# Kernel tuning notes

Measured on AMD Instinct MI355X. Metric: run time of the kernel, lower is better.

Reference implementation:

```python
import jax, jax.numpy as jnp
import numpy as np

B, S, D = 1, 2048, 4096
NH, NKV, HD = 32, 8, 128
ROPE_BASE = 500000.0
NEG = -1e30


def apply_rope(x):
    # x: [B, S, H, HD]; interleaved-pair rotary (Llama/torchtune style)
    pos = jnp.arange(x.shape[1], dtype=jnp.float32)
    inv_freq = ROPE_BASE ** (-jnp.arange(0, HD, 2, dtype=jnp.float32) / HD)  # [HD/2]
    ang = pos[:, None] * inv_freq[None, :]            # [S, HD/2]
    cos = jnp.cos(ang)[None, :, None, :]              # [1, S, 1, HD/2]
    sin = jnp.sin(ang)[None, :, None, :]
    xr = x.reshape(x.shape[0], x.shape[1], x.shape[2], HD // 2, 2)
    x0, x1 = xr[..., 0], xr[..., 1]
    out = jnp.stack([x0 * cos - x1 * sin, x0 * sin + x1 * cos], axis=-1)
    return out.reshape(x.shape).astype(x.dtype)


def setup_inputs() -> dict:
    key = jax.random.key(0)
    ks = jax.random.split(key, 5)
    sc = 1.0 / np.sqrt(D).astype(np.float32)
    return {
        "x": jax.random.normal(ks[0], (B, S, D), jnp.float32),
        "Wq": jax.random.normal(ks[1], (D, NH * HD), jnp.float32) * sc,
        "Wk": jax.random.normal(ks[2], (D, NKV * HD), jnp.float32) * sc,
        "Wv": jax.random.normal(ks[3], (D, NKV * HD), jnp.float32) * sc,
        "Wo": jax.random.normal(ks[4], (D, D), jnp.float32) * sc,
    }


def reference(x, Wq, Wk, Wv, Wo):
    # QKV projections (no bias; attention_bias=False)
    q = (x @ Wq).reshape(B, S, NH, HD)      # [B,S,NH,HD]
    k = (x @ Wk).reshape(B, S, NKV, HD)     # [B,S,NKV,HD]
    v = (x @ Wv).reshape(B, S, NKV, HD)
    # RoPE on q and k
    q = apply_rope(q)
    k = apply_rope(k)
    # GQA: group q heads over kv heads instead of materializing expanded k/v
    g = NH // NKV
    qg = q.reshape(B, S, NKV, g, HD)
    scale = 1.0 / np.sqrt(HD).astype(np.float32)
    scores = jnp.einsum('bsngh,btnh->bngst', qg, k) * scale  # [B,NKV,g,S,S]
    causal = jnp.tril(jnp.ones((S, S), dtype=bool))
    scores = jnp.where(causal, scores, NEG)
    p = jax.nn.softmax(scores, axis=-1)
    o = jnp.einsum('bngst,btnh->bsngh', p, v).reshape(B, S, NH * HD)
    return o @ Wo
```

## Files before the change

### kernel.cpp

```cpp
#include <hip/hip_runtime.h>
#include <cstdint>

#define S_LEN 2048
#define D_DIM 4096
#define NHEAD 32
#define NKVH  8
#define HDIM  128
#define NQKV  6144

typedef __bf16 bf16x8 __attribute__((ext_vector_type(8)));
typedef __bf16 bf16x2 __attribute__((ext_vector_type(2)));
typedef float floatx4 __attribute__((ext_vector_type(4)));
typedef unsigned short u16;
typedef unsigned int u32;

__device__ __forceinline__ u16 f2bf(float f) {
  u32 u = __builtin_bit_cast(u32, f);
  u += 0x7fffu + ((u >> 16) & 1u);
  return (u16)(u >> 16);
}
__device__ __forceinline__ float bf2f(u16 h) {
  u32 u = ((u32)h) << 16;
  return __builtin_bit_cast(float, u);
}
__device__ __forceinline__ u32 pack2(float a, float b) {
  bf16x2 t;
  t[0] = (__bf16)a;
  t[1] = (__bf16)b;
  return __builtin_bit_cast(u32, t);
}

__device__ __forceinline__ void gll16(const void* g, const void* l) {
  __builtin_amdgcn_global_load_lds(
      (const __attribute__((address_space(1))) u32*)(unsigned long long)(uintptr_t)g,
      (__attribute__((address_space(3))) u32*)(u32)(uintptr_t)l, 16, 0, 0);
}


__global__ __launch_bounds__(256) void prep_kernel(const float* __restrict__ x,
                                                   const float* __restrict__ Wq,
                                                   const float* __restrict__ Wk,
                                                   const float* __restrict__ Wv,
                                                   const float* __restrict__ Wo,
                                                   u16* __restrict__ x_bf,
                                                   u16* __restrict__ wqkvT,
                                                   u16* __restrict__ woT) {
  int id = blockIdx.x;
  if (id < 8192) {
    int i = (id * 256 + (int)threadIdx.x) * 4;
    float4 v = *(const float4*)(x + i);
    u32 lo = (u32)f2bf(v.x) | ((u32)f2bf(v.y) << 16);
    u32 hi = (u32)f2bf(v.z) | ((u32)f2bf(v.w) << 16);
    *(uint2*)(x_bf + i) = make_uint2(lo, hi);
    return;
  }
  id -= 8192;
  __shared__ float tile[64][65];
  const float* src;
  u16* dst;
  int N;
  if (id < 4096) {
    src = Wq; dst = wqkvT; N = 4096;
  } else if (id < 5120) {
    src = Wk; dst = wqkvT + (size_t)4096 * 4096; N = 1024; id -= 4096;
  } else if (id < 6144) {
    src = Wv; dst = wqkvT + (size_t)5120 * 4096; N = 1024; id -= 5120;
  } else {
    src = Wo; dst = woT; N = 4096; id -= 6144;
  }
  const int nb = id / 64, kb = id % 64;
  const int k0 = kb * 64, n0 = nb * 64;
  const int t = threadIdx.x;
  const int c4 = (t & 15) * 4, r0 = t >> 4;
#pragma unroll
  for (int p = 0; p < 4; ++p) {
    int r = r0 + p * 16;
    float4 v = *(const float4*)(src + (size_t)(k0 + r) * N + n0 + c4);
    tile[r][c4 + 0] = v.x;
    tile[r][c4 + 1] = v.y;
    tile[r][c4 + 2] = v.z;
    tile[r][c4 + 3] = v.w;
  }
  __syncthreads();
#pragma unroll
  for (int p = 0; p < 4; ++p) {
    int rr = r0 + p * 16;
    u32 a = (u32)f2bf(tile[c4 + 0][rr]) | ((u32)f2bf(tile[c4 + 1][rr]) << 16);
    u32 b = (u32)f2bf(tile[c4 + 2][rr]) | ((u32)f2bf(tile[c4 + 3][rr]) << 16);
    *(uint2*)(dst + (size_t)(n0 + rr) * 4096 + k0 + c4) = make_uint2(a, b);
  }
}


__global__ __launch_bounds__(256) void rope_vt_kernel(u16* __restrict__ qkv,
                                                      u16* __restrict__ vt) {
  int id = blockIdx.x;
  __shared__ u16 tile[64][65];
  if (id < 20480) {
    const int y = id >> 11, s = id & 2047;
    const int sub = threadIdx.x >> 6;
    const int i = threadIdx.x & 63;
    const int hh = y * 4 + sub;
    const int colbase = (hh < NHEAD) ? hh * HDIM : D_DIM + (hh - NHEAD) * HDIM;
    u32* p = (u32*)(qkv + (size_t)s * NQKV + colbase) + i;
    u32 pr = *p;
    float x0 = bf2f((u16)(pr & 0xffffu));
    float x1 = bf2f((u16)(pr >> 16));
    float invf = expf(-(float)(2 * i) * (13.122363377404328f / 128.0f));
    float ang = (float)s * invf;
    float cs = cosf(ang), sn = sinf(ang);
    float o0 = x0 * cs - x1 * sn;
    float o1 = x0 * sn + x1 * cs;
    *p = (u32)f2bf(o0) | ((u32)f2bf(o1) << 16);
    return;
  }
  const int vb = id - 20480;
  const int hk = vb >> 6;
  const int d0 = ((vb >> 5) & 1) * 64;
  const int s0 = (vb & 31) * 64;
  const int t = threadIdx.x, c = t & 63, r0 = t >> 6;
#pragma unroll
  for (int p = 0; p < 16; ++p) {
    int r = r0 + p * 4;
    tile[r][c] = qkv[(size_t)(s0 + r) * NQKV + 5120 + hk * HDIM + d0 + c];
  }
  __syncthreads();
#pragma unroll
  for (int p = 0; p < 16; ++p) {
    int rr = r0 + p * 4;
    vt[((size_t)hk * HDIM + d0 + rr) * S_LEN + s0 + c] = tile[c][rr];
  }
}


template <bool BF16_OUT>
__global__ __launch_bounds__(256) void gemm_bt(const u16* __restrict__ A,
                                               const u16* __restrict__ Bt,
                                               void* __restrict__ Cout,
                                               int M, int N, int K, int lda, int ldb) {
  __shared__ u16 As[2][128 * 32];
  __shared__ u16 Bs[2][128 * 32];
  const int tid = threadIdx.x;
  const int w = tid >> 6, lane = tid & 63;
  const int quad = lane >> 4, l15 = lane & 15;
  const int m0 = blockIdx.y * 128, n0 = blockIdx.x * 128;
  const int wm = (w & 1) * 64, wn = (w >> 1) * 64;
  floatx4 acc[4][4];
#pragma unroll
  for (int mi = 0; mi < 4; ++mi)
#pragma unroll
    for (int ni = 0; ni < 4; ++ni)
#pragma unroll
      for (int j = 0; j < 4; ++j) acc[mi][ni][j] = 0.0f;

  const int srow = w * 32 + (lane >> 2);
  const int kcol = (lane & 3) * 8;
  const u16* pA0 = A + (size_t)(m0 + srow) * lda + kcol;
  const u16* pA1 = pA0 + (size_t)16 * lda;
  const u16* pB0 = Bt + (size_t)(n0 + srow) * ldb + kcol;
  const u16* pB1 = pB0 + (size_t)16 * ldb;

  for (int k0 = 0; k0 < K; k0 += 64) {
#pragma unroll
    for (int c = 0; c < 2; ++c) {
      gll16(pA0 + k0 + c * 32, As[c] + (w * 32) * 32);
      gll16(pA1 + k0 + c * 32, As[c] + (w * 32 + 16) * 32);
      gll16(pB0 + k0 + c * 32, Bs[c] + (w * 32) * 32);
      gll16(pB1 + k0 + c * 32, Bs[c] + (w * 32 + 16) * 32);
    }
    __syncthreads();
#pragma unroll
    for (int c2 = 0; c2 < 2; ++c2) {
      bf16x8 a[4], b[4];
#pragma unroll
      for (int mi = 0; mi < 4; ++mi)
        a[mi] = *(const bf16x8*)(As[c2] + (wm + mi * 16 + l15) * 32 + quad * 8);
#pragma unroll
      for (int ni = 0; ni < 4; ++ni)
        b[ni] = *(const bf16x8*)(Bs[c2] + (wn + ni * 16 + l15) * 32 + quad * 8);
#pragma unroll
      for (int mi = 0; mi < 4; ++mi)
#pragma unroll
        for (int ni = 0; ni < 4; ++ni)
          acc[mi][ni] = __builtin_amdgcn_mfma_f32_16x16x32_bf16(a[mi], b[ni], acc[mi][ni], 0, 0, 0);
    }
    __syncthreads();
  }
#pragma unroll
  for (int mi = 0; mi < 4; ++mi)
#pragma unroll
    for (int ni = 0; ni < 4; ++ni) {
      int row = m0 + wm + mi * 16 + quad * 4;
      int col = n0 + wn + ni * 16 + l15;
#pragma unroll
      for (int j = 0; j < 4; ++j) {
        if (BF16_OUT)
          ((u16*)Cout)[(size_t)(row + j) * N + col] = f2bf(acc[mi][ni][j]);
        else
          ((float*)Cout)[(size_t)(row + j) * N + col] = acc[mi][ni][j];
      }
    }
}


__global__ __launch_bounds__(512, 4) void attn_kernel(const u16* __restrict__ qkv,
                                                      const u16* __restrict__ vt,
                                                      u16* __restrict__ attn_o) {
  __shared__ u16 Ks[2][64 * 128];
  __shared__ u16 Vs[2][128 * 64];
  __shared__ u16 Ps[8][16 * 64];
  const int tid = threadIdx.x, w = tid >> 6, lane = tid & 63;
  const int quad = lane >> 4, l15 = lane & 15;
  const int h = blockIdx.y, hk = h >> 2;
  const int bx = (h & 16) ? blockIdx.x : (gridDim.x - 1 - blockIdx.x);
  const int qb = bx * 128;
  const int mq0 = qb + w * 16;
  const int qrow = mq0 + l15;
  const float scale2 = 0.12751744591813488f;
  const int xsw = (l15 & 7) * 8;

  bf16x8 qfrag[4];
  {
    const u16* qp = qkv + (size_t)qrow * NQKV + h * HDIM + quad * 8;
#pragma unroll
    for (int c = 0; c < 4; ++c) qfrag[c] = *(const bf16x8*)(qp + c * 32);
  }

  floatx4 o[8];
#pragma unroll
  for (int nf = 0; nf < 8; ++nf)
#pragma unroll
    for (int j = 0; j < 4; ++j) o[nf][j] = 0.0f;
  float m_ = -1e30f, l_ = 0.0f;

  const int krow0 = w * 8 + (lane >> 4);
  const int krow1 = krow0 + 4;
  const int kcol0 = ((lane & 15) * 8) ^ ((krow0 & 7) * 8);
  const int kcol1 = ((lane & 15) * 8) ^ ((krow1 & 7) * 8);
  const u16* kg0 = qkv + (size_t)krow0 * NQKV + (D_DIM + hk * HDIM) + kcol0;
  const u16* kg1 = qkv + (size_t)krow1 * NQKV + (D_DIM + hk * HDIM) + kcol1;
  const int vd0 = w * 16 + (lane >> 3);
  const int vd1 = vd0 + 8;
  const int vcol = ((lane & 7) * 8) ^ (((lane >> 3) & 7) * 8);
  const u16* vg0 = vt + ((size_t)hk * HDIM + vd0) * S_LEN + vcol;
  const u16* vg1 = vt + ((size_t)hk * HDIM + vd1) * S_LEN + vcol;
  const int sofs0 = w * 1024 + lane * 8;
  const int sofs1 = sofs0 + 512;

  const int nkt = 2 * bx + 2;

#define STAGE(b, kb2)                                    \
  do {                                                   \
    gll16(kg0 + (size_t)(kb2)*NQKV, &Ks[b][sofs0]);      \
    gll16(kg1 + (size_t)(kb2)*NQKV, &Ks[b][sofs1]);      \
    gll16(vg0 + (kb2), &Vs[b][sofs0]);                   \
    gll16(vg1 + (kb2), &Vs[b][sofs1]);                   \
  } while (0)

  STAGE(0, 0);
  __syncthreads();

  for (int kt = 0; kt < nkt; ++kt) {
    const int kb = kt * 64;
    const int cur = kt & 1;
    if (kt + 1 < nkt) STAGE(cur ^ 1, kb + 64);

    if (kb <= mq0 + 15) {
      const u16* ksb = Ks[cur];
      const u16* vsb = Vs[cur];
      floatx4 sn[4];
#pragma unroll
      for (int ki = 0; ki < 4; ++ki)
#pragma unroll
        for (int j = 0; j < 4; ++j) sn[ki][j] = 0.0f;

      __builtin_amdgcn_s_setprio(1);
#pragma unroll
      for (int ki = 0; ki < 4; ++ki) {
        if (kb + ki * 16 <= mq0 + 15) {
#pragma unroll
          for (int c = 0; c < 4; ++c) {
            bf16x8 kf = *(const bf16x8*)(ksb + (ki * 16 + l15) * 128 + ((c * 32 + quad * 8) ^ xsw));
            sn[ki] = __builtin_amdgcn_mfma_f32_16x16x32_bf16(kf, qfrag[c], sn[ki], 0, 0, 0);
          }
        }
      }
      __builtin_amdgcn_s_setprio(0);

      float mv = -1e30f;
      if (kb + 63 <= mq0) {
#pragma unroll
        for (int ki = 0; ki < 4; ++ki)
#pragma unroll
          for (int j = 0; j < 4; ++j) mv = fmaxf(mv, sn[ki][j]);
      } else {
#pragma unroll
        for (int ki = 0; ki < 4; ++ki) {
          if (kb + ki * 16 <= mq0 + 15) {
#pragma unroll
            for (int j = 0; j < 4; ++j) {
              int key = kb + ki * 16 + quad * 4 + j;
              float s = (key <= qrow) ? sn[ki][j] : -1e30f;
              sn[ki][j] = s;
              mv = fmaxf(mv, s);
            }
          }
        }
      }
      mv = fmaxf(mv, __shfl_xor(mv, 16, 64));
      mv = fmaxf(mv, __shfl_xor(mv, 32, 64));

      const float THRR = 62.73636f;
      const bool skip = __all(mv <= m_ + THRR);
      float a_ = 1.0f, mb;
      if (skip) {
        mb = -m_ * scale2;
      } else {
        float mn = fmaxf(m_, mv);
        a_ = exp2f((m_ - mn) * scale2);
        m_ = mn;
        mb = -mn * scale2;
      }

      float ps = 0.0f;
      u16* psrow = &Ps[w][l15 * 64];
#pragma unroll
      for (int ki = 0; ki < 4; ++ki) {
        uint2 pk;
        if (kb + ki * 16 <= mq0 + 15) {
          float p0 = exp2f(fmaf(sn[ki][0], scale2, mb));
          float p1 = exp2f(fmaf(sn[ki][1], scale2, mb));
          float p2 = exp2f(fmaf(sn[ki][2], scale2, mb));
          float p3 = exp2f(fmaf(sn[ki][3], scale2, mb));
          ps += (p0 + p1) + (p2 + p3);
          pk.x = pack2(p0, p1);
          pk.y = pack2(p2, p3);
        } else {
          pk = make_uint2(0u, 0u);
        }
        *(uint2*)(psrow + ((ki * 16 + quad * 4) ^ xsw)) = pk;
      }
      ps += __shfl_xor(ps, 16, 64);
      ps += __shfl_xor(ps, 32, 64);

      if (skip) {
        l_ += ps;
      } else {
        l_ = l_ * a_ + ps;
        float al[4];
#pragma unroll
        for (int j = 0; j < 4; ++j) al[j] = __shfl(a_, quad * 4 + j, 16);
#pragma unroll
        for (int nf = 0; nf < 8; ++nf)
#pragma unroll
          for (int j = 0; j < 4; ++j) o[nf][j] *= al[j];
      }

      bf16x8 pa0 = *(const bf16x8*)(psrow + ((quad * 8) ^ xsw));
      bf16x8 pa1 = *(const bf16x8*)(psrow + ((32 + quad * 8) ^ xsw));

      __builtin_amdgcn_s_setprio(1);
#pragma unroll
      for (int nf = 0; nf < 8; ++nf) {
        const u16* vrow = vsb + (nf * 16 + l15) * 64;
        bf16x8 vb0 = *(const bf16x8*)(vrow + ((quad * 8) ^ xsw));
        bf16x8 vb1 = *(const bf16x8*)(vrow + ((32 + quad * 8) ^ xsw));
        o[nf] = __builtin_amdgcn_mfma_f32_16x16x32_bf16(pa0, vb0, o[nf], 0, 0, 0);
        o[nf] = __builtin_amdgcn_mfma_f32_16x16x32_bf16(pa1, vb1, o[nf], 0, 0, 0);
      }
      __builtin_amdgcn_s_setprio(0);
    }
    __syncthreads();
  }
#undef STAGE

  float linv = 1.0f / l_;
  float rl[4];
#pragma unroll
  for (int j = 0; j < 4; ++j) rl[j] = __shfl(linv, quad * 4 + j, 16);
#pragma unroll
  for (int nf = 0; nf < 8; ++nf)
#pragma unroll
    for (int j = 0; j < 4; ++j) {
      int row = mq0 + quad * 4 + j;
      int col = h * HDIM + nf * 16 + l15;
      attn_o[(size_t)row * D_DIM + col] = f2bf(o[nf][j] * rl[j]);
    }
}


extern "C" void kernel_launch(void* const* d_in, const int* in_sizes, int n_in,
                              void* d_out, int out_size, void* d_ws, size_t ws_size,
                              hipStream_t stream) {
  const float* x  = (const float*)d_in[0];
  const float* Wq = (const float*)d_in[1];
  const float* Wk = (const float*)d_in[2];
  const float* Wv = (const float*)d_in[3];
  const float* Wo = (const float*)d_in[4];
  float* out = (float*)d_out;
  char* ws = (char*)d_ws;
  const size_t MB = 1024 * 1024;
  u16* x_bf   = (u16*)(ws);
  u16* wqkvT  = (u16*)(ws + 16 * MB);
  u16* woT    = (u16*)(ws + 64 * MB);
  u16* qkv    = (u16*)(ws + 96 * MB);
  u16* vt     = (u16*)(ws + 120 * MB);
  u16* attn_o = (u16*)(ws + 124 * MB);

  prep_kernel<<<8192 + 10240, 256, 0, stream>>>(x, Wq, Wk, Wv, Wo, x_bf, wqkvT, woT);
  gemm_bt<true><<<dim3(48, 16), 256, 0, stream>>>(x_bf, wqkvT, qkv, S_LEN, NQKV, D_DIM, D_DIM, D_DIM);
  rope_vt_kernel<<<20480 + 512, 256, 0, stream>>>(qkv, vt);
  attn_kernel<<<dim3(S_LEN / 128, NHEAD), 512, 0, stream>>>(qkv, vt, attn_o);
  gemm_bt<false><<<dim3(32, 16), 256, 0, stream>>>(attn_o, woT, out, S_LEN, D_DIM, D_DIM, D_DIM, D_DIM);
}
```

Measured before the change: 496.3 us.

## Use 256x256-tile pipelined GEMM kernel for QKV projection

Adds a new bf16 GEMM kernel with 256x256 output tiles, 512 threads, double-buffered LDS with direct global-to-LDS loads, and a phased schedule that interleaves staging of the next tile with MFMA work under raised wave priority. The QKV projection now uses it in place of the 128x128-tile kernel. The goal is to raise data reuse per byte loaded and to overlap memory traffic with compute. The trade-off is that only 192 blocks are launched, fewer than the CU count, and heavy per-thread register use.

```diff
diff --git a/kernel.cpp b/kernel.cpp
--- a/kernel.cpp
+++ b/kernel.cpp
@@ -203,6 +203,119 @@
 }
 
 
+template <bool BF16_OUT>
+__global__ __launch_bounds__(512, 2) void gemm256_bt(const u16* __restrict__ A,
+                                                     const u16* __restrict__ Bt,
+                                                     void* __restrict__ Cout,
+                                                     int M, int N, int K, int lda, int ldb) {
+  __shared__ u16 Ab[2][16384];
+  __shared__ u16 Bb[2][16384];
+  const int tid = threadIdx.x;
+  const int w = tid >> 6, lane = tid & 63;
+  const int quad = lane >> 4, l15 = lane & 15;
+  const int wr = w >> 2, wc = w & 3;
+  const int m0 = blockIdx.y * 256, n0 = blockIdx.x * 256;
+  const int xsw = (l15 & 7) * 8;
+
+  floatx4 acc[8][4];
+#pragma unroll
+  for (int mf = 0; mf < 8; ++mf)
+#pragma unroll
+    for (int nf = 0; nf < 4; ++nf)
+#pragma unroll
+      for (int j = 0; j < 4; ++j) acc[mf][nf][j] = 0.0f;
+
+  const int srow = tid >> 3;
+  const int scol = ((tid & 7) * 8) ^ ((srow & 7) * 8);
+  const u16* gA = A + (size_t)(m0 + srow) * lda + scol;
+  const u16* gB = Bt + (size_t)(n0 + srow) * ldb + scol;
+
+#define SA(buf, h, tt)                                                                       \
+  do {                                                                                       \
+    gll16(gA + (size_t)((h)*128) * lda + (size_t)(tt)*64, &Ab[buf][(h)*8192 + w * 512]);     \
+    gll16(gA + (size_t)((h)*128 + 64) * lda + (size_t)(tt)*64,                               \
+          &Ab[buf][(h)*8192 + 4096 + w * 512]);                                              \
+  } while (0)
+#define SB(buf, h, tt)                                                                       \
+  do {                                                                                       \
+    gll16(gB + (size_t)((h)*128) * ldb + (size_t)(tt)*64, &Bb[buf][(h)*8192 + w * 512]);     \
+    gll16(gB + (size_t)((h)*128 + 64) * ldb + (size_t)(tt)*64,                               \
+          &Bb[buf][(h)*8192 + 4096 + w * 512]);                                              \
+  } while (0)
+
+  SA(0, 0, 0);
+  SA(0, 1, 0);
+  SB(0, 0, 0);
+  SB(0, 1, 0);
+  SB(1, 0, 1);
+  SB(1, 1, 1);
+  asm volatile("s_waitcnt vmcnt(4)" ::: "memory");
+  __builtin_amdgcn_s_barrier();
+
+  const int NT = K >> 6;
+  bf16x8 bfr[4][2];
+
+#define GPH(AC, BC, MPAIR, LOADB, STAGEOP, VM)                                               \
+  {                                                                                          \
+    if (LOADB) {                                                                             \
+      _Pragma("unroll") for (int nf = 0; nf < 4; ++nf)                                       \
+        _Pragma("unroll") for (int kc = 0; kc < 2; ++kc)                                     \
+          bfr[nf][kc] = *(const bf16x8*)((BC) + (wc * 64 + nf * 16 + l15) * 64 +             \
+                                         ((kc * 32 + quad * 8) ^ xsw));                      \
+    }                                                                                        \
+    bf16x8 af[2][2];                                                                         \
+    _Pragma("unroll") for (int mi = 0; mi < 2; ++mi)                                         \
+      _Pragma("unroll") for (int kc = 0; kc < 2; ++kc)                                       \
+        af[mi][kc] = *(const bf16x8*)((AC) + (wr * 128 + ((MPAIR)*2 + mi) * 16 + l15) * 64 + \
+                                      ((kc * 32 + quad * 8) ^ xsw));                         \
+    STAGEOP;                                                                                 \
+    __builtin_amdgcn_sched_barrier(0);                                                       \
+    __builtin_amdgcn_s_barrier();                                                            \
+    asm volatile("s_waitcnt lgkmcnt(0)" ::: "memory");                                       \
+    __builtin_amdgcn_sched_barrier(0);                                                       \
+    __builtin_amdgcn_s_setprio(1);                                                           \
+    _Pragma("unroll") for (int mi = 0; mi < 2; ++mi)                                         \
+      _Pragma("unroll") for (int nf = 0; nf < 4; ++nf)                                       \
+        _Pragma("unroll") for (int kc = 0; kc < 2; ++kc)                                     \
+          acc[(MPAIR)*2 + mi][nf] = __builtin_amdgcn_mfma_f32_16x16x32_bf16(                 \
+              af[mi][kc], bfr[nf][kc], acc[(MPAIR)*2 + mi][nf], 0, 0, 0);                    \
+    __builtin_amdgcn_s_setprio(0);                                                           \
+    if (VM) asm volatile("s_waitcnt vmcnt(4)" ::: "memory");                                 \
+    __builtin_amdgcn_s_barrier();                                                            \
+  }
+
+  for (int t = 0; t < NT; t += 2) {
+    const bool stg = (t + 2 < NT);
+    GPH(Ab[0], Bb[0], 0, true,  { SA(1, 0, t + 1); }, false)
+    GPH(Ab[0], Bb[0], 1, false, { SA(1, 1, t + 1); }, false)
+    GPH(Ab[0], Bb[0], 2, false, { if (stg) SB(0, 0, t + 2); }, false)
+    GPH(Ab[0], Bb[0], 3, false, { if (stg) SB(0, 1, t + 2); }, true)
+    GPH(Ab[1], Bb[1], 0, true,  { if (stg) SA(0, 0, t + 2); }, false)
+    GPH(Ab[1], Bb[1], 1, false, { if (stg) SA(0, 1, t + 2); }, false)
+    GPH(Ab[1], Bb[1], 2, false, { if (stg) SB(1, 0, t + 3); }, false)
+    GPH(Ab[1], Bb[1], 3, false, { if (stg) SB(1, 1, t + 3); }, true)
+  }
+#undef GPH
+#undef SA
+#undef SB
+
+#pragma unroll
+  for (int mf = 0; mf < 8; ++mf)
+#pragma unroll
+    for (int nf = 0; nf < 4; ++nf) {
+      int row = m0 + wr * 128 + mf * 16 + quad * 4;
+      int col = n0 + wc * 64 + nf * 16 + l15;
+#pragma unroll
+      for (int j = 0; j < 4; ++j) {
+        if (BF16_OUT)
+          ((u16*)Cout)[(size_t)(row + j) * N + col] = f2bf(acc[mf][nf][j]);
+        else
+          ((float*)Cout)[(size_t)(row + j) * N + col] = acc[mf][nf][j];
+      }
+    }
+}
+
+
 __global__ __launch_bounds__(512, 4) void attn_kernel(const u16* __restrict__ qkv,
                                                       const u16* __restrict__ vt,
                                                       u16* __restrict__ attn_o) {
@@ -408,7 +521,7 @@
   u16* attn_o = (u16*)(ws + 124 * MB);
 
   prep_kernel<<<8192 + 10240, 256, 0, stream>>>(x, Wq, Wk, Wv, Wo, x_bf, wqkvT, woT);
-  gemm_bt<true><<<dim3(48, 16), 256, 0, stream>>>(x_bf, wqkvT, qkv, S_LEN, NQKV, D_DIM, D_DIM, D_DIM);
+  gemm256_bt<true><<<dim3(24, 8), 512, 0, stream>>>(x_bf, wqkvT, qkv, S_LEN, NQKV, D_DIM, D_DIM, D_DIM);
   rope_vt_kernel<<<20480 + 512, 256, 0, stream>>>(qkv, vt);
   attn_kernel<<<dim3(S_LEN / 128, NHEAD), 512, 0, stream>>>(qkv, vt, attn_o);
   gemm_bt<false><<<dim3(32, 16), 256, 0, stream>>>(attn_o, woT, out, S_LEN, D_DIM, D_DIM, D_DIM, D_DIM);
```

New measurement: 479.9 us. 1.03x faster.

## Replace 128x128 GEMM with 256-row 8-wave pipelined GEMM with swizzled LDS

Applied to the files above, without the earlier changes.

Replaces the 128x128 four-wave bf16 GEMM with a 512-thread kernel that computes 256xBN tiles (BN=256 for the QKV projection, 128 for the output projection). A and B tiles are staged through XOR-swizzled LDS, double-buffered with 64-wide K steps. Global loads are interleaved between MFMA phases using explicit barriers, vmcnt/lgkmcnt waits and setprio. The goal is more reuse per loaded byte, fewer LDS bank conflicts, and overlap of memory traffic with matrix-core work. The cost is heavy register pressure from the 8xNF16 accumulators and fragile hand scheduling, and the QKV grid shrinks to 192 blocks, which may leave CUs idle.

```diff
diff --git a/kernel.cpp b/kernel.cpp
--- a/kernel.cpp
+++ b/kernel.cpp
@@ -133,71 +133,159 @@
 }
 
 
-template <bool BF16_OUT>
-__global__ __launch_bounds__(256) void gemm_bt(const u16* __restrict__ A,
-                                               const u16* __restrict__ Bt,
-                                               void* __restrict__ Cout,
-                                               int M, int N, int K, int lda, int ldb) {
-  __shared__ u16 As[2][128 * 32];
-  __shared__ u16 Bs[2][128 * 32];
+template <int NF16, bool BF16_OUT>
+__global__ __launch_bounds__(512, 2) void gemm256p(const u16* __restrict__ A,
+                                                   const u16* __restrict__ Bt,
+                                                   void* __restrict__ Cout,
+                                                   int M, int N, int K, int lda, int ldb) {
+  constexpr int WN = NF16 * 16;
+  constexpr int BN = 4 * WN;
+  __shared__ u16 Ab[2][16384];
+  __shared__ u16 Bb[2][BN * 64];
   const int tid = threadIdx.x;
   const int w = tid >> 6, lane = tid & 63;
   const int quad = lane >> 4, l15 = lane & 15;
-  const int m0 = blockIdx.y * 128, n0 = blockIdx.x * 128;
-  const int wm = (w & 1) * 64, wn = (w >> 1) * 64;
-  floatx4 acc[4][4];
-#pragma unroll
-  for (int mi = 0; mi < 4; ++mi)
-#pragma unroll
-    for (int ni = 0; ni < 4; ++ni)
-#pragma unroll
-      for (int j = 0; j < 4; ++j) acc[mi][ni][j] = 0.0f;
-
-  const int srow = w * 32 + (lane >> 2);
-  const int kcol = (lane & 3) * 8;
-  const u16* pA0 = A + (size_t)(m0 + srow) * lda + kcol;
-  const u16* pA1 = pA0 + (size_t)16 * lda;
-  const u16* pB0 = Bt + (size_t)(n0 + srow) * ldb + kcol;
-  const u16* pB1 = pB0 + (size_t)16 * ldb;
-
-  for (int k0 = 0; k0 < K; k0 += 64) {
-#pragma unroll
-    for (int c = 0; c < 2; ++c) {
-      gll16(pA0 + k0 + c * 32, As[c] + (w * 32) * 32);
-      gll16(pA1 + k0 + c * 32, As[c] + (w * 32 + 16) * 32);
-      gll16(pB0 + k0 + c * 32, Bs[c] + (w * 32) * 32);
-      gll16(pB1 + k0 + c * 32, Bs[c] + (w * 32 + 16) * 32);
+  const int wr = w >> 2, wc = w & 3;
+  const int m0 = blockIdx.y * 256, n0 = blockIdx.x * BN;
+  const int xsw = (l15 & 7) * 8;
+
+  floatx4 acc[8][NF16];
+#pragma unroll
+  for (int mf = 0; mf < 8; ++mf)
+#pragma unroll
+    for (int nf = 0; nf < NF16; ++nf)
+#pragma unroll
+      for (int j = 0; j < 4; ++j) acc[mf][nf][j] = 0.0f;
+
+  const int srow = tid >> 3;
+  const int scol = ((tid & 7) * 8) ^ ((srow & 7) * 8);
+  const u16* gA = A + (size_t)(m0 + srow) * lda + scol;
+  const u16* gB = Bt + (size_t)(n0 + srow) * ldb + scol;
+
+#define SA(buf, h, tt)                                                                         \
+  do {                                                                                         \
+    gll16(gA + (size_t)((h)*128) * lda + (size_t)(tt)*64, &Ab[buf][(h)*8192 + w * 512]);       \
+    gll16(gA + (size_t)((h)*128 + 64) * lda + (size_t)(tt)*64,                                 \
+          &Ab[buf][(h)*8192 + 4096 + w * 512]);                                                \
+  } while (0)
+#define SB(buf, h, tt)                                                                         \
+  do {                                                                                         \
+    gll16(gB + (size_t)((h)*128) * ldb + (size_t)(tt)*64, &Bb[buf][(h)*8192 + w * 512]);       \
+    gll16(gB + (size_t)((h)*128 + 64) * ldb + (size_t)(tt)*64,                                 \
+          &Bb[buf][(h)*8192 + 4096 + w * 512]);                                                \
+  } while (0)
+
+#define RD_B(BC)                                                                               \
+  _Pragma("unroll") for (int nf = 0; nf < NF16; ++nf)                                          \
+    _Pragma("unroll") for (int kc = 0; kc < 2; ++kc)                                           \
+      bfr[nf][kc] = *(const bf16x8*)((BC) + (wc * WN + nf * 16 + l15) * 64 +                   \
+                                     ((kc * 32 + quad * 8) ^ xsw));
+#define RD_A(DST, AC, MP)                                                                      \
+  _Pragma("unroll") for (int mi = 0; mi < 2; ++mi)                                             \
+    _Pragma("unroll") for (int kc = 0; kc < 2; ++kc)                                           \
+      (DST)[mi][kc] = *(const bf16x8*)((AC) + (wr * 128 + ((MP)*2 + mi) * 16 + l15) * 64 +     \
+                                       ((kc * 32 + quad * 8) ^ xsw));
+#define MM(MP, SRC)                                                                            \
+  __builtin_amdgcn_s_setprio(1);                                                               \
+  _Pragma("unroll") for (int mi = 0; mi < 2; ++mi)                                             \
+    _Pragma("unroll") for (int nf = 0; nf < NF16; ++nf)                                        \
+      _Pragma("unroll") for (int kc = 0; kc < 2; ++kc)                                         \
+        acc[(MP)*2 + mi][nf] = __builtin_amdgcn_mfma_f32_16x16x32_bf16(                        \
+            (SRC)[mi][kc], bfr[nf][kc], acc[(MP)*2 + mi][nf], 0, 0, 0);                        \
+  __builtin_amdgcn_s_setprio(0);
+#define LGKM0                                                                                  \
+  asm volatile("s_waitcnt lgkmcnt(0)" ::: "memory");                                           \
+  __builtin_amdgcn_sched_barrier(0);
+#define SBAR                                                                                   \
+  __builtin_amdgcn_sched_barrier(0);                                                           \
+  __builtin_amdgcn_s_barrier();
+#define VMGATE                                                                                 \
+  if (NF16 == 4) { asm volatile("s_waitcnt vmcnt(4)" ::: "memory"); }                          \
+  else           { asm volatile("s_waitcnt vmcnt(2)" ::: "memory"); }
+
+  SA(0, 0, 0);
+  SA(0, 1, 0);
+  SB(0, 0, 0);
+  if (NF16 == 4) SB(0, 1, 0);
+  SB(1, 0, 1);
+  if (NF16 == 4) SB(1, 1, 1);
+  VMGATE;
+
+  const int NT = K >> 6;
+  bf16x8 bfr[NF16][2], afA[2][2], afB[2][2];
+
+  for (int t = 0; t < NT; t += 2) {
+    const bool s2 = (t + 2 < NT), s3 = (t + 3 < NT);
+    SBAR;
+    RD_B(Bb[0]);
+    RD_A(afA, Ab[0], 0);
+    LGKM0;
+    MM(0, afA);
+    RD_A(afB, Ab[0], 1);
+    SA(1, 0, t + 1);
+    SBAR;
+    LGKM0;
+    MM(1, afB);
+    RD_A(afA, Ab[0], 2);
+    SA(1, 1, t + 1);
+    SBAR;
+    LGKM0;
+    MM(2, afA);
+    RD_A(afB, Ab[0], 3);
+    if (s2) SB(0, 0, t + 2);
+    SBAR;
+    LGKM0;
+    MM(3, afB);
+    if (NF16 == 4) {
+      if (s2) SB(0, 1, t + 2);
     }
-    __syncthreads();
-#pragma unroll
-    for (int c2 = 0; c2 < 2; ++c2) {
-      bf16x8 a[4], b[4];
-#pragma unroll
-      for (int mi = 0; mi < 4; ++mi)
-        a[mi] = *(const bf16x8*)(As[c2] + (wm + mi * 16 + l15) * 32 + quad * 8);
-#pragma unroll
-      for (int ni = 0; ni < 4; ++ni)
-        b[ni] = *(const bf16x8*)(Bs[c2] + (wn + ni * 16 + l15) * 32 + quad * 8);
-#pragma unroll
-      for (int mi = 0; mi < 4; ++mi)
-#pragma unroll
-        for (int ni = 0; ni < 4; ++ni)
-          acc[mi][ni] = __builtin_amdgcn_mfma_f32_16x16x32_bf16(a[mi], b[ni], acc[mi][ni], 0, 0, 0);
+    VMGATE;
+    SBAR;
+    RD_B(Bb[1]);
+    RD_A(afA, Ab[1], 0);
+    LGKM0;
+    MM(0, afA);
+    RD_A(afB, Ab[1], 1);
+    if (s2) SA(0, 0, t + 2);
+    SBAR;
+    LGKM0;
+    MM(1, afB);
+    RD_A(afA, Ab[1], 2);
+    if (s2) SA(0, 1, t + 2);
+    SBAR;
+    LGKM0;
+    MM(2, afA);
+    RD_A(afB, Ab[1], 3);
+    if (s3) SB(1, 0, t + 3);
+    SBAR;
+    LGKM0;
+    MM(3, afB);
+    if (NF16 == 4) {
+      if (s3) SB(1, 1, t + 3);
     }
-    __syncthreads();
-  }
-#pragma unroll
-  for (int mi = 0; mi < 4; ++mi)
-#pragma unroll
-    for (int ni = 0; ni < 4; ++ni) {
-      int row = m0 + wm + mi * 16 + quad * 4;
-      int col = n0 + wn + ni * 16 + l15;
+    VMGATE;
+  }
+#undef SA
+#undef SB
+#undef RD_B
+#undef RD_A
+#undef MM
+#undef LGKM0
+#undef SBAR
+#undef VMGATE
+
+#pragma unroll
+  for (int mf = 0; mf < 8; ++mf)
+#pragma unroll
+    for (int nf = 0; nf < NF16; ++nf) {
+      int row = m0 + wr * 128 + mf * 16 + quad * 4;
+      int col = n0 + wc * WN + nf * 16 + l15;
 #pragma unroll
       for (int j = 0; j < 4; ++j) {
         if (BF16_OUT)
-          ((u16*)Cout)[(size_t)(row + j) * N + col] = f2bf(acc[mi][ni][j]);
+          ((u16*)Cout)[(size_t)(row + j) * N + col] = f2bf(acc[mf][nf][j]);
         else
-          ((float*)Cout)[(size_t)(row + j) * N + col] = acc[mi][ni][j];
+          ((float*)Cout)[(size_t)(row + j) * N + col] = acc[mf][nf][j];
       }
     }
 }
@@ -408,8 +496,8 @@
   u16* attn_o = (u16*)(ws + 124 * MB);
 
   prep_kernel<<<8192 + 10240, 256, 0, stream>>>(x, Wq, Wk, Wv, Wo, x_bf, wqkvT, woT);
-  gemm_bt<true><<<dim3(48, 16), 256, 0, stream>>>(x_bf, wqkvT, qkv, S_LEN, NQKV, D_DIM, D_DIM, D_DIM);
+  gemm256p<4, true><<<dim3(24, 8), 512, 0, stream>>>(x_bf, wqkvT, qkv, S_LEN, NQKV, D_DIM, D_DIM, D_DIM);
   rope_vt_kernel<<<20480 + 512, 256, 0, stream>>>(qkv, vt);
   attn_kernel<<<dim3(S_LEN / 128, NHEAD), 512, 0, stream>>>(qkv, vt, attn_o);
-  gemm_bt<false><<<dim3(32, 16), 256, 0, stream>>>(attn_o, woT, out, S_LEN, D_DIM, D_DIM, D_DIM, D_DIM);
-}
+  gemm256p<2, false><<<dim3(32, 8), 512, 0, stream>>>(attn_o, woT, out, S_LEN, D_DIM, D_DIM, D_DIM, D_DIM);
+}
```

New measurement: 453.7 us. 1.09x faster.
